# Kernel optimization log

Hardware: AMD Instinct MI355X
Metric: run time of the kernel (lower is better)

The kernel has to match this reference:

```python
import jax, jax.numpy as jnp
import numpy as np
import math

D_MODEL = 1024
N_HEADS = 16
Q_PROJ = D_MODEL // 4
KV_PROJ = D_MODEL // 4
DH = D_MODEL // N_HEADS
LN_EPS = 1e-5


def _layernorm(x, gamma, beta):
    mu = jnp.mean(x, axis=-1, keepdims=True)
    var = jnp.mean(jnp.square(x - mu), axis=-1, keepdims=True)
    return (x - mu) * jax.lax.rsqrt(var + LN_EPS) * gamma + beta


def setup_inputs() -> dict:
    key = jax.random.key(0)
    ks = jax.random.split(key, 7)
    B, S = 2, 2048
    x = jax.random.normal(ks[0], (B, S, D_MODEL), dtype=jnp.float32)
    W_dq = 0.01 * jax.random.normal(ks[1], (D_MODEL, Q_PROJ), dtype=jnp.float32)
    W_uq = 0.01 * jax.random.normal(ks[2], (Q_PROJ, D_MODEL), dtype=jnp.float32)
    W_dkv = 0.01 * jax.random.normal(ks[3], (D_MODEL, KV_PROJ), dtype=jnp.float32)
    W_ukv = 0.01 * jax.random.normal(ks[4], (KV_PROJ, 2 * D_MODEL), dtype=jnp.float32)
    W_o = 0.01 * jax.random.normal(ks[5], (D_MODEL, D_MODEL), dtype=jnp.float32)
    return {
        "x": x,
        "W_dq": W_dq, "W_uq": W_uq,
        "q_ln_g": jnp.ones((Q_PROJ,), jnp.float32), "q_ln_b": jnp.zeros((Q_PROJ,), jnp.float32),
        "W_dkv": W_dkv, "W_ukv": W_ukv,
        "kv_ln_g": jnp.ones((KV_PROJ,), jnp.float32), "kv_ln_b": jnp.zeros((KV_PROJ,), jnp.float32),
        "W_o": W_o,
    }


def reference(x, W_dq, W_uq, q_ln_g, q_ln_b, W_dkv, W_ukv, kv_ln_g, kv_ln_b, W_o):
    B, S, D = x.shape
    # low-rank Q path
    cq = _layernorm(x @ W_dq, q_ln_g, q_ln_b)          # [B,S,q_proj]
    Q = cq @ W_uq                                       # [B,S,D]
    # low-rank KV path
    ckv = _layernorm(x @ W_dkv, kv_ln_g, kv_ln_b)       # [B,S,kv_proj]
    KV = ckv @ W_ukv                                    # [B,S,2D]
    K, V = KV[..., :D], KV[..., D:]
    q = Q.reshape(B, S, N_HEADS, DH)
    k = K.reshape(B, S, N_HEADS, DH)
    v = V.reshape(B, S, N_HEADS, DH)
    scores = jnp.einsum("bqhd,bkhd->bhqk", q, k) / math.sqrt(float(DH))
    # faithful to original: multiply by tril mask, then set exact zeros to -inf
    mask = jnp.tril(jnp.ones((S, S), dtype=scores.dtype))
    scores = scores * mask
    scores = jnp.where(scores == 0, -jnp.inf, scores)
    attn = jax.nn.softmax(scores, axis=-1)
    out = jnp.einsum("bhqk,bkhd->bqhd", attn, v).reshape(B, S, D)
    return out @ W_o.T
```

## Files before the change

kernel.cpp:

```cpp
#include <hip/hip_runtime.h>

typedef __bf16 bf16;
typedef __bf16 bf16x4 __attribute__((ext_vector_type(4)));
typedef __bf16 bf16x8 __attribute__((ext_vector_type(8)));
typedef float f32x4 __attribute__((ext_vector_type(4)));

#define D_MODEL 1024
#define PROJ    256
#define SEQ     2048
#define BATCH   2
#define TOK     4096
#define NH      16
#define DH      64
#define NEG_BIG (-1e30f)
#define QSCALE  0.18033688011112042f

#if __has_builtin(__builtin_amdgcn_exp2f)
#define EXP2(x) __builtin_amdgcn_exp2f(x)
#else
#define EXP2(x) exp2f(x)
#endif

typedef __attribute__((address_space(3))) unsigned int  lds_u32;
typedef __attribute__((address_space(1))) unsigned int  glb_u32;

__device__ __forceinline__ void gl2lds16(const void* gsrc, void* ldst) {
    __builtin_amdgcn_global_load_lds((const glb_u32*)gsrc, (lds_u32*)ldst, 16, 0, 0);
}

template <int CTRL>
__device__ __forceinline__ float dppmov(float x) {
    int i = __builtin_bit_cast(int, x);
    i = __builtin_amdgcn_update_dpp(i, i, CTRL, 0xf, 0xf, false);
    return __builtin_bit_cast(float, i);
}
__device__ __forceinline__ float rowsum16(float v) {
    v += dppmov<0xB1>(v);
    v += dppmov<0x4E>(v);
    v += dppmov<0x141>(v);
    v += dppmov<0x140>(v);
    return v;
}

__global__ void prep_weights_kernel(
    const float* __restrict__ W_o,  const float* __restrict__ W_dq,
    const float* __restrict__ W_dkv, const float* __restrict__ W_uq,
    const float* __restrict__ W_ukv, const float* __restrict__ x,
    bf16* __restrict__ Wo16, bf16* __restrict__ Wt_dq, bf16* __restrict__ Wt_dkv,
    bf16* __restrict__ Wt_uq, bf16* __restrict__ Wt_ukv, bf16* __restrict__ x16) {
    const int R0 = 1048576;
    const int R1 = R0 + 262144;
    const int R2 = R1 + 262144;
    const int R3 = R2 + 262144;
    const int R4 = R3 + 524288;
    const int R5 = R4 + 4194304;
    for (int i = blockIdx.x * blockDim.x + threadIdx.x; i < R5;
         i += gridDim.x * blockDim.x) {
        if (i < R0) {
            Wo16[i] = (bf16)W_o[i];
        } else if (i < R1) {
            int j = i - R0, n = j >> 10, k = j & 1023;
            Wt_dq[j] = (bf16)W_dq[k * 256 + n];
        } else if (i < R2) {
            int j = i - R1, n = j >> 10, k = j & 1023;
            Wt_dkv[j] = (bf16)W_dkv[k * 256 + n];
        } else if (i < R3) {
            int j = i - R2, n = j >> 8, k = j & 255;
            Wt_uq[j] = (bf16)W_uq[k * 1024 + n];
        } else if (i < R4) {
            int j = i - R3, n = j >> 8, k = j & 255;
            Wt_ukv[j] = (bf16)W_ukv[k * 2048 + n];
        } else {
            int j = i - R4;
            x16[j] = (bf16)x[j];
        }
    }
}

__global__ __launch_bounds__(256) void gemm_ln_kernel(
    const bf16* __restrict__ x16,
    const bf16* __restrict__ Wt_q, const bf16* __restrict__ Wt_kv,
    const float* __restrict__ q_g, const float* __restrict__ q_b,
    const float* __restrict__ kv_g, const float* __restrict__ kv_b,
    bf16* __restrict__ cq, bf16* __restrict__ ckv) {
    __shared__ alignas(16) bf16 xA[32 * 32];
    __shared__ alignas(16) bf16 wB[256 * 32];
    __shared__ float red1[4][16];
    __shared__ float red2[4][16];

    const int K = 1024;
    const bf16* Wt = blockIdx.y ? Wt_kv : Wt_q;
    const float* gamma = blockIdx.y ? kv_g : q_g;
    const float* beta  = blockIdx.y ? kv_b : q_b;
    bf16* out = blockIdx.y ? ckv : cq;

    const int m0 = blockIdx.x * 32;
    const int wv = threadIdx.x >> 6;
    const int lane = threadIdx.x & 63;
    const int g = lane >> 4;
    const int ln16 = lane & 15;
    const int wr = wv >> 1;
    const int wc = wv & 1;

    const int crow = lane >> 2;
    const int ckc = lane & 3;
    const bf16* gx = x16 + (size_t)(m0 + (wv & 1) * 16 + crow) * K + ckc * 8;
    char* lx = (char*)xA + (wv & 1) * 1024;
    const bf16* gw = Wt + (size_t)(64 * wv + crow) * K + ckc * 8;
    char* lw = (char*)wB + wv * 4096;

    f32x4 acc[8] = {};
    for (int k0 = 0; k0 < K; k0 += 32) {
        if (wv < 2) gl2lds16(gx + k0, lx);
#pragma unroll
        for (int i = 0; i < 4; ++i)
            gl2lds16(gw + (size_t)i * 16 * K + k0, lw + i * 1024);
        __syncthreads();

        bf16x8 a = *(const bf16x8*)(xA + (wr * 16 + ln16) * 32 + g * 8);
#pragma unroll
        for (int t = 0; t < 8; ++t) {
            bf16x8 b = *(const bf16x8*)(wB + (wc * 128 + 16 * t + ln16) * 32 + g * 8);
            acc[t] = __builtin_amdgcn_mfma_f32_16x16x32_bf16(a, b, acc[t], 0, 0, 0);
        }
        __syncthreads();
    }

    float s1[4], s2[4];
#pragma unroll
    for (int r = 0; r < 4; ++r) {
        float a = 0.f, b = 0.f;
#pragma unroll
        for (int t = 0; t < 8; ++t) { float v = acc[t][r]; a += v; b += v * v; }
        s1[r] = rowsum16(a); s2[r] = rowsum16(b);
    }
    if (ln16 == 0) {
#pragma unroll
        for (int r = 0; r < 4; ++r) {
            red1[wv][g * 4 + r] = s1[r];
            red2[wv][g * 4 + r] = s2[r];
        }
    }
    __syncthreads();
#pragma unroll
    for (int r = 0; r < 4; ++r) {
        int rl = g * 4 + r;
        float t1 = red1[wr * 2][rl] + red1[wr * 2 + 1][rl];
        float t2 = red2[wr * 2][rl] + red2[wr * 2 + 1][rl];
        float mu = t1 * (1.0f / 256.0f);
        float var = t2 * (1.0f / 256.0f) - mu * mu;
        float rs = rsqrtf(var + 1e-5f);
        int row = m0 + wr * 16 + rl;
#pragma unroll
        for (int t = 0; t < 8; ++t) {
            int col = wc * 128 + 16 * t + ln16;
            float v = (acc[t][r] - mu) * rs * gamma[col] + beta[col];
            out[(size_t)row * PROJ + col] = (bf16)v;
        }
    }
}

template <typename OutT>
__device__ __forceinline__ void gemm_body(
    const bf16* __restrict__ A, const bf16* __restrict__ Bt,
    OutT* __restrict__ C, bf16* __restrict__ C2, int N, int K,
    int bx, int by, int mode, bf16* tA, bf16* tB) {
    const int w = threadIdx.x >> 6;
    const int lane = threadIdx.x & 63;
    const int g = lane >> 4;
    const int ln16 = lane & 15;
    const int wr = w >> 1;
    const int wc = w & 1;

    const int m0 = bx * 64;
    const int n0 = by * 128;

    const int crow = lane >> 2;
    const int ckc = lane & 3;
    const bf16* gA  = A  + (size_t)(m0 + w * 16 + crow) * K + ckc * 8;
    const bf16* gB0 = Bt + (size_t)(n0 + w * 16 + crow) * K + ckc * 8;
    const bf16* gB1 = Bt + (size_t)(n0 + 64 + w * 16 + crow) * K + ckc * 8;
    char* lA  = (char*)tA + w * 1024;
    char* lB0 = (char*)tB + w * 1024;
    char* lB1 = (char*)tB + 4096 + w * 1024;

    f32x4 acc[2][4] = {};
    for (int k0 = 0; k0 < K; k0 += 32) {
        gl2lds16(gA + k0, lA);
        gl2lds16(gB0 + k0, lB0);
        gl2lds16(gB1 + k0, lB1);
        __syncthreads();

        bf16x8 af[2], bf[4];
#pragma unroll
        for (int s = 0; s < 2; ++s)
            af[s] = *(const bf16x8*)(tA + (wr * 32 + s * 16 + ln16) * 32 + g * 8);
#pragma unroll
        for (int t = 0; t < 4; ++t)
            bf[t] = *(const bf16x8*)(tB + (wc * 64 + t * 16 + ln16) * 32 + g * 8);
#pragma unroll
        for (int s = 0; s < 2; ++s)
#pragma unroll
            for (int t = 0; t < 4; ++t)
                acc[s][t] = __builtin_amdgcn_mfma_f32_16x16x32_bf16(
                    af[s], bf[t], acc[s][t], 0, 0, 0);
        __syncthreads();
    }

#pragma unroll
    for (int s = 0; s < 2; ++s)
#pragma unroll
        for (int t = 0; t < 4; ++t) {
            const int col = n0 + wc * 64 + t * 16 + ln16;
            const int tok0 = m0 + wr * 32 + s * 16 + g * 4;
            if (mode == 2 && col >= 1024) {
                int cc = col - 1024;
                int h = cc >> 6, d = cc & 63;
                int b = tok0 >> 11, sq = tok0 & 2047;
                bf16x4 pk;
#pragma unroll
                for (int r = 0; r < 4; ++r) pk[r] = (bf16)acc[s][t][r];
                *(bf16x4*)(C2 + ((size_t)((b * 16 + h) * 64 + d) * SEQ + sq)) = pk;
            } else {
#pragma unroll
                for (int r = 0; r < 4; ++r) {
                    int row = tok0 + r;
                    float v = acc[s][t][r];
                    if (mode == 0) {
                        C[(size_t)row * N + col] = (OutT)v;
                    } else {
                        if (mode == 1) v *= QSCALE;
                        int h = col >> 6, d = col & 63;
                        int b = row >> 11, sq = row & 2047;
                        C[((size_t)((b * 16 + h) * 2048 + sq)) * 64 + d] = (OutT)v;
                    }
                }
            }
        }
}

__global__ __launch_bounds__(256) void gemm_o_kernel(
    const bf16* __restrict__ A, const bf16* __restrict__ Bt,
    float* __restrict__ C, int M, int N, int K) {
    __shared__ alignas(16) bf16 tA[64 * 32];
    __shared__ alignas(16) bf16 tB[128 * 32];
    gemm_body<float>(A, Bt, C, nullptr, N, K, blockIdx.x, blockIdx.y, 0, tA, tB);
}

__global__ __launch_bounds__(256) void gemm_qkv_kernel(
    const bf16* __restrict__ cq, const bf16* __restrict__ Wt_uq,
    const bf16* __restrict__ ckv, const bf16* __restrict__ Wt_ukv,
    bf16* __restrict__ Qh, bf16* __restrict__ Kh, bf16* __restrict__ Vt) {
    __shared__ alignas(16) bf16 tA[64 * 32];
    __shared__ alignas(16) bf16 tB[128 * 32];
    const int i = blockIdx.x;
    if (i < 512) {
        gemm_body<bf16>(cq, Wt_uq, Qh, nullptr, D_MODEL, PROJ,
                        i >> 3, i & 7, 1, tA, tB);
    } else {
        const int j = i - 512;
        gemm_body<bf16>(ckv, Wt_ukv, Kh, Vt, 2 * D_MODEL, PROJ,
                        j >> 4, j & 15, 2, tA, tB);
    }
}

__device__ __forceinline__ void qk_exp_pack(
    int k0, int q, bool masked, int g, int ln16,
    bf16x8 aq0, bf16x8 aq1, const bf16x8* Kf,
    float& li, bf16x8& P1, bf16x8& P2) {
    f32x4 sc[4];
#pragma unroll
    for (int c = 0; c < 4; ++c) {
        f32x4 z = {};
        z = __builtin_amdgcn_mfma_f32_16x16x32_bf16(Kf[2 * c], aq0, z, 0, 0, 0);
        z = __builtin_amdgcn_mfma_f32_16x16x32_bf16(Kf[2 * c + 1], aq1, z, 0, 0, 0);
        sc[c] = z;
    }
    if (masked) {
        const int kb = k0 + 8 * g;
#pragma unroll
        for (int c = 0; c < 4; ++c)
#pragma unroll
            for (int r = 0; r < 4; ++r) {
                int kcol = kb + (c & 1) * 4 + r + ((c >> 1) << 5);
                if (kcol > q) sc[c][r] = NEG_BIG;
            }
    }
#pragma unroll
    for (int c = 0; c < 4; ++c)
#pragma unroll
        for (int r = 0; r < 4; ++r) {
            float p = EXP2(sc[c][r]);
            sc[c][r] = p;
            li += p;
        }
#pragma unroll
    for (int r = 0; r < 4; ++r) {
        P1[r] = (bf16)sc[0][r]; P1[4 + r] = (bf16)sc[1][r];
        P2[r] = (bf16)sc[2][r]; P2[4 + r] = (bf16)sc[3][r];
    }
}

__device__ __forceinline__ void pv_accum(
    bf16x8 P1, bf16x8 P2, const bf16x8* Vf, f32x4* o) {
#pragma unroll
    for (int t = 0; t < 4; ++t) {
        o[t] = __builtin_amdgcn_mfma_f32_16x16x32_bf16(Vf[2 * t], P1, o[t], 0, 0, 0);
        o[t] = __builtin_amdgcn_mfma_f32_16x16x32_bf16(Vf[2 * t + 1], P2, o[t], 0, 0, 0);
    }
}

__global__ __launch_bounds__(256, 2) void attn_kernel(
    const bf16* __restrict__ Qh, const bf16* __restrict__ Kh,
    const bf16* __restrict__ Vt, bf16* __restrict__ AT) {
    __shared__ alignas(16) bf16 kbuf[64 * 64];
    __shared__ alignas(16) bf16 vbuf[64 * 64];

    const int lane = threadIdx.x & 63;
    const int g = lane >> 4;
    const int ln16 = lane & 15;
    const int wv = threadIdx.x >> 6;

    const int bh = blockIdx.x & 31;
    const int qsuper = 31 - (blockIdx.x >> 5);
    const int qb = qsuper * 64 + wv * 16;
    const int q = qb + ln16;
    const int ntiles = qsuper + 1;

    const bf16* Kbh = Kh + (size_t)bh * SEQ * DH;
    const bf16* Vbh = Vt + (size_t)bh * DH * SEQ;

    const bf16* qp = Qh + ((size_t)bh * SEQ + q) * DH + g * 8;
    bf16x8 aq0 = *(const bf16x8*)qp, aq1 = *(const bf16x8*)(qp + 32);

    f32x4 o[4] = {};
    float li = 0.f;

    char* kd0 = (char*)kbuf + wv * 2048;
    char* kd1 = kd0 + 1024;
    char* vd0 = (char*)vbuf + wv * 2048;
    char* vd1 = vd0 + 1024;
    const int rho = lane >> 3;
    const int sl  = lane & 7;
    const int c0 = sl ^ (rho & 3);
    const int c1 = sl ^ ((rho & 3) | 4);
    const int kofs0 = (16 * wv + rho) * 64 + c0 * 8;
    const int kofs1 = (16 * wv + 8 + rho) * 64 + c1 * 8;
    const size_t vrow0 = (size_t)(16 * wv + rho) * SEQ;
    const size_t vrow1 = (size_t)(16 * wv + 8 + rho) * SEQ;
    const int vc0 = c0 * 8, vc1 = c1 * 8;

    const int row_base = ((ln16 & 12) << 1) + (ln16 & 3);
    const bf16* kr[4];
#pragma unroll
    for (int c = 0; c < 4; ++c) {
        const int row = row_base + (c & 1) * 4 + ((c >> 1) << 5);
        const int fr = (row & 3) | (((row >> 3) & 1) << 2);
        kr[c] = kbuf + row * 64 + ((g ^ fr) * 8);
    }
    const bf16* vr[4];
#pragma unroll
    for (int t = 0; t < 4; ++t) {
        const int d = 16 * t + ln16;
        const int fd = (d & 3) | (((d >> 3) & 1) << 2);
        vr[t] = vbuf + d * 64 + ((g ^ fd) * 8);
    }

    for (int kt = 0; kt < ntiles; ++kt) {
        const int k0 = kt * 64;
        gl2lds16(Kbh + (size_t)k0 * 64 + kofs0, kd0);
        gl2lds16(Kbh + (size_t)k0 * 64 + kofs1, kd1);
        gl2lds16(Vbh + vrow0 + k0 + vc0, vd0);
        gl2lds16(Vbh + vrow1 + k0 + vc1, vd1);
        __syncthreads();

        bf16x8 Kf[8], Vf[8];
#pragma unroll
        for (int c = 0; c < 4; ++c) {
            Kf[2 * c]     = *(const bf16x8*)(kr[c]);
            Kf[2 * c + 1] = *(const bf16x8*)((const bf16*)((size_t)kr[c] ^ 64));
        }
#pragma unroll
        for (int t = 0; t < 4; ++t) {
            Vf[2 * t]     = *(const bf16x8*)(vr[t]);
            Vf[2 * t + 1] = *(const bf16x8*)((const bf16*)((size_t)vr[t] ^ 64));
        }

        bf16x8 P1, P2;
        qk_exp_pack(k0, q, kt == qsuper, g, ln16, aq0, aq1, Kf, li, P1, P2);
        pv_accum(P1, P2, Vf, o);
        __syncthreads();
    }

    li += __shfl_xor(li, 16); li += __shfl_xor(li, 32);
    float inv = 1.0f / li;

    const int b = bh >> 4, h = bh & 15;
    const size_t tok = (size_t)(b * SEQ + q) * D_MODEL + h * DH;
#pragma unroll
    for (int t = 0; t < 4; ++t) {
        bf16x4 pk;
#pragma unroll
        for (int r = 0; r < 4; ++r) pk[r] = (bf16)(o[t][r] * inv);
        *(bf16x4*)(AT + tok + 16 * t + 4 * g) = pk;
    }
}

extern "C" void kernel_launch(void* const* d_in, const int* in_sizes, int n_in,
                              void* d_out, int out_size, void* d_ws, size_t ws_size,
                              hipStream_t stream) {
    const float* x     = (const float*)d_in[0];
    const float* W_dq  = (const float*)d_in[1];
    const float* W_uq  = (const float*)d_in[2];
    const float* q_g   = (const float*)d_in[3];
    const float* q_b   = (const float*)d_in[4];
    const float* W_dkv = (const float*)d_in[5];
    const float* W_ukv = (const float*)d_in[6];
    const float* kv_g  = (const float*)d_in[7];
    const float* kv_b  = (const float*)d_in[8];
    const float* W_o   = (const float*)d_in[9];

    char* ws = (char*)d_ws;
    size_t off = 0;
    bf16* Wo16   = (bf16*)(ws + off); off += (size_t)D_MODEL * D_MODEL * 2;
    bf16* Wt_dq  = (bf16*)(ws + off); off += (size_t)PROJ * D_MODEL * 2;
    bf16* Wt_dkv = (bf16*)(ws + off); off += (size_t)PROJ * D_MODEL * 2;
    bf16* Wt_uq  = (bf16*)(ws + off); off += (size_t)D_MODEL * PROJ * 2;
    bf16* Wt_ukv = (bf16*)(ws + off); off += (size_t)(2 * D_MODEL) * PROJ * 2;
    bf16* x16    = (bf16*)(ws + off); off += (size_t)TOK * D_MODEL * 2;
    bf16* cq     = (bf16*)(ws + off); off += (size_t)TOK * PROJ * 2;
    bf16* ckv    = (bf16*)(ws + off); off += (size_t)TOK * PROJ * 2;
    bf16* Qh     = (bf16*)(ws + off); off += (size_t)TOK * D_MODEL * 2;
    bf16* Kh     = (bf16*)(ws + off); off += (size_t)TOK * D_MODEL * 2;
    bf16* Vt     = (bf16*)(ws + off); off += (size_t)TOK * D_MODEL * 2;
    bf16* AT     = (bf16*)(ws + off); off += (size_t)TOK * D_MODEL * 2;

    prep_weights_kernel<<<2048, 256, 0, stream>>>(
        W_o, W_dq, W_dkv, W_uq, W_ukv, x,
        Wo16, Wt_dq, Wt_dkv, Wt_uq, Wt_ukv, x16);

    gemm_ln_kernel<<<dim3(TOK / 32, 2), 256, 0, stream>>>(
        x16, Wt_dq, Wt_dkv, q_g, q_b, kv_g, kv_b, cq, ckv);

    gemm_qkv_kernel<<<1536, 256, 0, stream>>>(cq, Wt_uq, ckv, Wt_ukv, Qh, Kh, Vt);

    attn_kernel<<<1024, 256, 0, stream>>>(Qh, Kh, Vt, AT);

    gemm_o_kernel<<<dim3(TOK / 64, D_MODEL / 128), 256, 0, stream>>>(
        AT, Wo16, (float*)d_out, TOK, D_MODEL, D_MODEL);
}
```

Measured before the change: 190.8 us.

## Double-buffer attention K/V tiles, pair causal q-blocks, two q-tiles per wave

```diff
diff --git a/kernel.cpp b/kernel.cpp
--- a/kernel.cpp
+++ b/kernel.cpp
@@ -310,11 +310,11 @@
     }
 }
 
-__global__ __launch_bounds__(256, 2) void attn_kernel(
+__global__ __launch_bounds__(128) void attn_kernel(
     const bf16* __restrict__ Qh, const bf16* __restrict__ Kh,
     const bf16* __restrict__ Vt, bf16* __restrict__ AT) {
-    __shared__ alignas(16) bf16 kbuf[64 * 64];
-    __shared__ alignas(16) bf16 vbuf[64 * 64];
+    __shared__ alignas(128) bf16 kbuf[2][64 * 64];
+    __shared__ alignas(128) bf16 vbuf[2][64 * 64];
 
     const int lane = threadIdx.x & 63;
     const int g = lane >> 4;
@@ -322,87 +322,120 @@
     const int wv = threadIdx.x >> 6;
 
     const int bh = blockIdx.x & 31;
-    const int qsuper = 31 - (blockIdx.x >> 5);
-    const int qb = qsuper * 64 + wv * 16;
-    const int q = qb + ln16;
-    const int ntiles = qsuper + 1;
+    const int pr = blockIdx.x >> 5;
 
     const bf16* Kbh = Kh + (size_t)bh * SEQ * DH;
     const bf16* Vbh = Vt + (size_t)bh * DH * SEQ;
 
-    const bf16* qp = Qh + ((size_t)bh * SEQ + q) * DH + g * 8;
-    bf16x8 aq0 = *(const bf16x8*)qp, aq1 = *(const bf16x8*)(qp + 32);
-
-    f32x4 o[4] = {};
-    float li = 0.f;
-
-    char* kd0 = (char*)kbuf + wv * 2048;
-    char* kd1 = kd0 + 1024;
-    char* vd0 = (char*)vbuf + wv * 2048;
-    char* vd1 = vd0 + 1024;
     const int rho = lane >> 3;
     const int sl  = lane & 7;
-    const int c0 = sl ^ (rho & 3);
-    const int c1 = sl ^ ((rho & 3) | 4);
-    const int kofs0 = (16 * wv + rho) * 64 + c0 * 8;
-    const int kofs1 = (16 * wv + 8 + rho) * 64 + c1 * 8;
-    const size_t vrow0 = (size_t)(16 * wv + rho) * SEQ;
-    const size_t vrow1 = (size_t)(16 * wv + 8 + rho) * SEQ;
-    const int vc0 = c0 * 8, vc1 = c1 * 8;
+    int kofs[4];
+    size_t vofs[4];
+#pragma unroll
+    for (int i = 0; i < 4; ++i) {
+        const int row = 32 * wv + 8 * i + rho;
+        const int c = sl ^ ((rho & 3) | ((i & 1) << 2));
+        kofs[i] = row * 64 + c * 8;
+        vofs[i] = (size_t)row * SEQ + c * 8;
+    }
 
     const int row_base = ((ln16 & 12) << 1) + (ln16 & 3);
-    const bf16* kr[4];
+    int kro[4], vro[4];
 #pragma unroll
     for (int c = 0; c < 4; ++c) {
         const int row = row_base + (c & 1) * 4 + ((c >> 1) << 5);
         const int fr = (row & 3) | (((row >> 3) & 1) << 2);
-        kr[c] = kbuf + row * 64 + ((g ^ fr) * 8);
-    }
-    const bf16* vr[4];
+        kro[c] = row * 128 + (g ^ fr) * 16;
+    }
 #pragma unroll
     for (int t = 0; t < 4; ++t) {
         const int d = 16 * t + ln16;
         const int fd = (d & 3) | (((d >> 3) & 1) << 2);
-        vr[t] = vbuf + d * 64 + ((g ^ fd) * 8);
-    }
-
-    for (int kt = 0; kt < ntiles; ++kt) {
-        const int k0 = kt * 64;
-        gl2lds16(Kbh + (size_t)k0 * 64 + kofs0, kd0);
-        gl2lds16(Kbh + (size_t)k0 * 64 + kofs1, kd1);
-        gl2lds16(Vbh + vrow0 + k0 + vc0, vd0);
-        gl2lds16(Vbh + vrow1 + k0 + vc1, vd1);
+        vro[t] = d * 128 + (g ^ fd) * 16;
+    }
+
+    const int b = bh >> 4, h = bh & 15;
+
+    for (int ph = 0; ph < 2; ++ph) {
+        const int super = ph ? pr : 31 - pr;
+        const int nt = super + 1;
+        const int qb = super * 64 + wv * 32;
+
+        bf16x8 aq[2][2];
+#pragma unroll
+        for (int hh = 0; hh < 2; ++hh) {
+            const bf16* qp =
+                Qh + ((size_t)bh * SEQ + qb + 16 * hh + ln16) * DH + g * 8;
+            aq[hh][0] = *(const bf16x8*)qp;
+            aq[hh][1] = *(const bf16x8*)(qp + 32);
+        }
+
+        f32x4 o0[4] = {}, o1[4] = {};
+        float li0 = 0.f, li1 = 0.f;
+
+#pragma unroll
+        for (int i = 0; i < 4; ++i) {
+            gl2lds16(Kbh + kofs[i], (char*)kbuf + wv * 4096 + i * 1024);
+            gl2lds16(Vbh + vofs[i], (char*)vbuf + wv * 4096 + i * 1024);
+        }
         __syncthreads();
 
-        bf16x8 Kf[8], Vf[8];
-#pragma unroll
-        for (int c = 0; c < 4; ++c) {
-            Kf[2 * c]     = *(const bf16x8*)(kr[c]);
-            Kf[2 * c + 1] = *(const bf16x8*)((const bf16*)((size_t)kr[c] ^ 64));
-        }
+        int cur = 0;
+        for (int kt = 0; kt < nt; ++kt) {
+            if (kt + 1 < nt) {
+                const size_t k0n = (size_t)(kt + 1) * 64;
+                char* kb = (char*)kbuf + (cur ^ 1) * 8192 + wv * 4096;
+                char* vb = (char*)vbuf + (cur ^ 1) * 8192 + wv * 4096;
+#pragma unroll
+                for (int i = 0; i < 4; ++i) {
+                    gl2lds16(Kbh + k0n * 64 + kofs[i], kb + i * 1024);
+                    gl2lds16(Vbh + vofs[i] + k0n, vb + i * 1024);
+                }
+            }
+
+            const char* kb = (const char*)kbuf + cur * 8192;
+            const char* vb = (const char*)vbuf + cur * 8192;
+            bf16x8 Kf[8], Vf[8];
+#pragma unroll
+            for (int c = 0; c < 4; ++c) {
+                Kf[2 * c]     = *(const bf16x8*)(kb + kro[c]);
+                Kf[2 * c + 1] = *(const bf16x8*)(kb + (kro[c] ^ 64));
+            }
+#pragma unroll
+            for (int t = 0; t < 4; ++t) {
+                Vf[2 * t]     = *(const bf16x8*)(vb + vro[t]);
+                Vf[2 * t + 1] = *(const bf16x8*)(vb + (vro[t] ^ 64));
+            }
+
+            const int k0 = kt * 64;
+            const bool msk = (kt == super);
+            bf16x8 P1a, P2a, P1b, P2b;
+            qk_exp_pack(k0, qb + ln16, msk, g, ln16,
+                        aq[0][0], aq[0][1], Kf, li0, P1a, P2a);
+            qk_exp_pack(k0, qb + 16 + ln16, msk, g, ln16,
+                        aq[1][0], aq[1][1], Kf, li1, P1b, P2b);
+            pv_accum(P1a, P2a, Vf, o0);
+            pv_accum(P1b, P2b, Vf, o1);
+            __syncthreads();
+            cur ^= 1;
+        }
+
+        li0 += __shfl_xor(li0, 16); li0 += __shfl_xor(li0, 32);
+        li1 += __shfl_xor(li1, 16); li1 += __shfl_xor(li1, 32);
+        const float inv0 = 1.0f / li0, inv1 = 1.0f / li1;
+        const size_t tok0 = (size_t)(b * SEQ + qb + ln16) * D_MODEL + h * DH;
+        const size_t tok1 = (size_t)(b * SEQ + qb + 16 + ln16) * D_MODEL + h * DH;
 #pragma unroll
         for (int t = 0; t < 4; ++t) {
-            Vf[2 * t]     = *(const bf16x8*)(vr[t]);
-            Vf[2 * t + 1] = *(const bf16x8*)((const bf16*)((size_t)vr[t] ^ 64));
-        }
-
-        bf16x8 P1, P2;
-        qk_exp_pack(k0, q, kt == qsuper, g, ln16, aq0, aq1, Kf, li, P1, P2);
-        pv_accum(P1, P2, Vf, o);
-        __syncthreads();
-    }
-
-    li += __shfl_xor(li, 16); li += __shfl_xor(li, 32);
-    float inv = 1.0f / li;
-
-    const int b = bh >> 4, h = bh & 15;
-    const size_t tok = (size_t)(b * SEQ + q) * D_MODEL + h * DH;
-#pragma unroll
-    for (int t = 0; t < 4; ++t) {
-        bf16x4 pk;
-#pragma unroll
-        for (int r = 0; r < 4; ++r) pk[r] = (bf16)(o[t][r] * inv);
-        *(bf16x4*)(AT + tok + 16 * t + 4 * g) = pk;
+            bf16x4 pk0, pk1;
+#pragma unroll
+            for (int r = 0; r < 4; ++r) {
+                pk0[r] = (bf16)(o0[t][r] * inv0);
+                pk1[r] = (bf16)(o1[t][r] * inv1);
+            }
+            *(bf16x4*)(AT + tok0 + 16 * t + 4 * g) = pk0;
+            *(bf16x4*)(AT + tok1 + 16 * t + 4 * g) = pk1;
+        }
     }
 }
 
@@ -444,7 +477,7 @@
 
     gemm_qkv_kernel<<<1536, 256, 0, stream>>>(cq, Wt_uq, ckv, Wt_ukv, Qh, Kh, Vt);
 
-    attn_kernel<<<1024, 256, 0, stream>>>(Qh, Kh, Vt, AT);
+    attn_kernel<<<512, 128, 0, stream>>>(Qh, Kh, Vt, AT);
 
     gemm_o_kernel<<<dim3(TOK / 64, D_MODEL / 128), 256, 0, stream>>>(
         AT, Wo16, (float*)d_out, TOK, D_MODEL, D_MODEL);
```

Measured after the change: 205.5 us. 1.08x slower.
